# Performance work log

Hardware: AMD Instinct MI355X
Metric: run time of the kernel (lower is better)

The kernel has to match this reference:

```python
import jax, jax.numpy as jnp
import numpy as np

N_NODES = 100_000
N_EDGES = 1_600_000
RBF_DIM = 128
DIM = 64
N_CLUSTERS = 10
DIFF_RATE = 0.2


def softplus_sp(x):
    # torch.nn.Softplus(beta=0.5, threshold=14): (1/beta)*log(1+exp(beta*x)),
    # exact identity when beta*x > threshold
    bx = 0.5 * x
    return jnp.where(bx > 14.0, x, 2.0 * jnp.logaddexp(0.0, bx))


def setup_inputs() -> dict:
    key = jax.random.key(0)
    ks = jax.random.split(key, 9)
    rbf = jax.random.normal(ks[0], (N_EDGES, RBF_DIM), dtype=jnp.float32)
    new_node = jax.random.normal(ks[1], (N_NODES, DIM), dtype=jnp.float32)
    src = jax.random.randint(ks[2], (N_EDGES,), 0, N_NODES, dtype=jnp.int32)
    dst = jax.random.randint(ks[3], (N_EDGES,), 0, N_NODES, dtype=jnp.int32)
    cluster_id = jax.random.randint(ks[4], (N_NODES,), 0, N_CLUSTERS, dtype=jnp.int32)
    # intra-cluster edges always kept; inter-cluster (diff) edges sampled at diff_rate
    same = cluster_id[src] == cluster_id[dst]
    keep_diff = jax.random.uniform(ks[5], (N_EDGES,)) < DIFF_RATE
    edge_mask = same | ((~same) & keep_diff)
    # Linear params stored as [in, out]; equivalent to torch Linear weight.T
    W1 = jax.random.normal(ks[6], (RBF_DIM, DIM), dtype=jnp.float32) * 0.05
    b1 = jnp.zeros((DIM,), dtype=jnp.float32)
    W2 = jax.random.normal(ks[7], (DIM, DIM), dtype=jnp.float32) * 0.05
    b2 = jnp.zeros((DIM,), dtype=jnp.float32)
    return {"rbf": rbf, "new_node": new_node, "src": src, "dst": dst,
            "edge_mask": edge_mask, "W1": W1, "b1": b1, "W2": W2, "b2": b2}


def reference(rbf, new_node, src, dst, edge_mask, W1, b1, W2, b2):
    n_nodes = new_node.shape[0]
    # edge MLP applied to ALL edges (apply_edges runs on whole graph)
    h = softplus_sp(rbf @ W1 + b1) @ W2 + b2            # [E, dim]
    # gather src features, multiply by edge filter, mask to selected edges
    msg = jnp.where(edge_mask[:, None], new_node[src] * h, 0.0)  # [E, dim]
    # scatter-sum into destination nodes (nodes w/o messages get 0)
    out = jax.ops.segment_sum(msg, dst, num_segments=n_nodes)    # [N, dim]
    return out
```

## Files before the change

kernel.cpp:

```cpp
#include <hip/hip_runtime.h>
#include <hip/hip_bf16.h>

#define NN      100000
#define NE      1600000
#define RBF     128
#define DIM     64

__device__ __forceinline__ float lo_bf(unsigned int u) {
    union { unsigned int i; float f; } v; v.i = u << 16; return v.f;
}
__device__ __forceinline__ float hi_bf(unsigned int u) {
    union { unsigned int i; float f; } v; v.i = u & 0xffff0000u; return v.f;
}
__device__ __forceinline__ float us_bf(unsigned short u) {
    union { unsigned int i; float f; } v; v.i = ((unsigned int)u) << 16; return v.f;
}

__global__ void sniff_kernel(const unsigned int* __restrict__ rbf_raw,
                             const unsigned int* __restrict__ mask_raw,
                             int* __restrict__ flags)
{
    const int lane = threadIdx.x & 63;
    int fh = 0, mh = 0;
    for (int i = lane; i < 256; i += 64) {
        const unsigned int u = rbf_raw[i];
        if (((u >> 7) & 0xffu) >= 0x90u) fh = 1;
        if (mask_raw[i] > 1u) mh = 1;
    }
    const int fcnt = __popcll(__ballot(fh));
    const int mcnt = __popcll(__ballot(mh));
    if (lane == 0) {
        flags[0] = (fcnt >= 4) ? 1 : 0;
        flags[1] = (mcnt >= 4) ? 1 : 0;
    }
}

template <bool FP32>
__global__ __launch_bounds__(256, 2)
void edge_kernel(const void* __restrict__ rbf_v,
                 const void* __restrict__ nn_v,
                 const int*  __restrict__ src,
                 const int*  __restrict__ dst,
                 const void* __restrict__ mask_v,
                 const void* __restrict__ W1_v,
                 const void* __restrict__ b1_v,
                 const void* __restrict__ W2_v,
                 const void* __restrict__ b2_v,
                 const int*  __restrict__ flags,
                 float*      __restrict__ acc)
{
    if ((flags[0] != 0) != FP32) return;
    const int mask8 = flags[1];

    const int lane = threadIdx.x & 63;
    const int wib  = threadIdx.x >> 6;
    const int gw   = blockIdx.x * 4 + wib;
    const int nw   = gridDim.x * 4;

    float w1c[RBF];
    float w2c[DIM];
    float b1v, b2v;
    if constexpr (FP32) {
        const float* W1 = (const float*)W1_v;
        const float* W2 = (const float*)W2_v;
#pragma unroll
        for (int k = 0; k < RBF; ++k) w1c[k] = W1[k * DIM + lane];
#pragma unroll
        for (int j = 0; j < DIM; ++j) w2c[j] = W2[j * DIM + lane];
        b1v = ((const float*)b1_v)[lane];
        b2v = ((const float*)b2_v)[lane];
    } else {
        const unsigned short* W1 = (const unsigned short*)W1_v;
        const unsigned short* W2 = (const unsigned short*)W2_v;
#pragma unroll
        for (int k = 0; k < RBF; ++k) w1c[k] = us_bf(W1[k * DIM + lane]);
#pragma unroll
        for (int j = 0; j < DIM; ++j) w2c[j] = us_bf(W2[j * DIM + lane]);
        b1v = us_bf(((const unsigned short*)b1_v)[lane]);
        b2v = us_bf(((const unsigned short*)b2_v)[lane]);
    }

    __shared__ alignas(16) float sp_lds[4][DIM];
    float* myl = sp_lds[wib];

    for (int base = gw * 64; base < NE; base += nw * 64) {
        const int e_l = base + lane;
        int m_l;
        if (mask8) m_l = ((const unsigned char*)mask_v)[e_l];
        else       m_l = ((const int*)mask_v)[e_l];
        const int s_l = src[e_l];
        const int d_l = dst[e_l];
        unsigned long long bal = __ballot(m_l != 0);

        while (bal) {
            const int l = __ffsll((unsigned long long)bal) - 1;
            bal &= bal - 1;
            const int ee = __builtin_amdgcn_readfirstlane(base + l);
            const int s  = __shfl(s_l, l);
            const int d  = __shfl(d_l, l);

            float a0 = b1v, a1 = 0.f, a2 = 0.f, a3 = 0.f;
            if constexpr (FP32) {
                const float4* r = (const float4*)((const float*)rbf_v + (size_t)ee * RBF);
#pragma unroll
                for (int q = 0; q < RBF / 4; q += 4) {
                    const float4 v0 = r[q + 0], v1 = r[q + 1];
                    const float4 v2 = r[q + 2], v3 = r[q + 3];
                    a0 += v0.x*w1c[4*q+ 0] + v0.y*w1c[4*q+ 1] + v0.z*w1c[4*q+ 2] + v0.w*w1c[4*q+ 3];
                    a1 += v1.x*w1c[4*q+ 4] + v1.y*w1c[4*q+ 5] + v1.z*w1c[4*q+ 6] + v1.w*w1c[4*q+ 7];
                    a2 += v2.x*w1c[4*q+ 8] + v2.y*w1c[4*q+ 9] + v2.z*w1c[4*q+10] + v2.w*w1c[4*q+11];
                    a3 += v3.x*w1c[4*q+12] + v3.y*w1c[4*q+13] + v3.z*w1c[4*q+14] + v3.w*w1c[4*q+15];
                }
            } else {
                const unsigned int* r = (const unsigned int*)rbf_v + (size_t)ee * (RBF / 2);
#pragma unroll
                for (int k2 = 0; k2 < RBF / 2; k2 += 4) {
                    const unsigned int u0 = r[k2 + 0], u1 = r[k2 + 1];
                    const unsigned int u2 = r[k2 + 2], u3 = r[k2 + 3];
                    a0 += lo_bf(u0) * w1c[2*k2 + 0] + hi_bf(u0) * w1c[2*k2 + 1];
                    a1 += lo_bf(u1) * w1c[2*k2 + 2] + hi_bf(u1) * w1c[2*k2 + 3];
                    a2 += lo_bf(u2) * w1c[2*k2 + 4] + hi_bf(u2) * w1c[2*k2 + 5];
                    a3 += lo_bf(u3) * w1c[2*k2 + 6] + hi_bf(u3) * w1c[2*k2 + 7];
                }
            }
            const float x = (a0 + a1) + (a2 + a3);

            const float bx = 0.5f * x;
            float sp;
            if (bx > 14.0f) sp = x;
            else sp = 2.0f * (fmaxf(bx, 0.0f) + log1pf(__expf(-fabsf(bx))));

            myl[lane] = sp;
            __builtin_amdgcn_wave_barrier();
            const float4* spv = (const float4*)myl;
            float h0 = b2v, h1 = 0.f, h2 = 0.f, h3 = 0.f;
#pragma unroll
            for (int j4 = 0; j4 < DIM / 4; j4 += 4) {
                const float4 v0 = spv[j4 + 0], v1 = spv[j4 + 1];
                const float4 v2 = spv[j4 + 2], v3 = spv[j4 + 3];
                h0 += v0.x*w2c[4*j4+ 0] + v0.y*w2c[4*j4+ 1] + v0.z*w2c[4*j4+ 2] + v0.w*w2c[4*j4+ 3];
                h1 += v1.x*w2c[4*j4+ 4] + v1.y*w2c[4*j4+ 5] + v1.z*w2c[4*j4+ 6] + v1.w*w2c[4*j4+ 7];
                h2 += v2.x*w2c[4*j4+ 8] + v2.y*w2c[4*j4+ 9] + v2.z*w2c[4*j4+10] + v2.w*w2c[4*j4+11];
                h3 += v3.x*w2c[4*j4+12] + v3.y*w2c[4*j4+13] + v3.z*w2c[4*j4+14] + v3.w*w2c[4*j4+15];
            }
            const float h = (h0 + h1) + (h2 + h3);
            __builtin_amdgcn_wave_barrier();

            float nnv;
            if constexpr (FP32) nnv = ((const float*)nn_v)[(size_t)s * DIM + lane];
            else                nnv = us_bf(((const unsigned short*)nn_v)[(size_t)s * DIM + lane]);
            atomicAdd(&acc[(size_t)d * DIM + lane], nnv * h);
        }
    }
}

__global__ void finalize_kernel(const float* __restrict__ acc,
                                void* __restrict__ out,
                                const int* __restrict__ flags, int n)
{
    const int i = blockIdx.x * blockDim.x + threadIdx.x;
    if (i < n) {
        const float v = acc[i];
        if (flags[0]) ((float*)out)[i] = v;
        else          ((__hip_bfloat16*)out)[i] = __float2bfloat16(v);
    }
}

extern "C" void kernel_launch(void* const* d_in, const int* in_sizes, int n_in,
                              void* d_out, int out_size, void* d_ws, size_t ws_size,
                              hipStream_t stream)
{
    const void* rbf  = d_in[0];
    const void* nn   = d_in[1];
    const int*  src  = (const int*)d_in[2];
    const int*  dst  = (const int*)d_in[3];
    const void* mask = d_in[4];
    const void* W1   = d_in[5];
    const void* b1   = d_in[6];
    const void* W2   = d_in[7];
    const void* b2   = d_in[8];

    int*   flags = (int*)d_ws;
    float* acc   = (float*)d_ws + 64;

    hipMemsetAsync(acc, 0, (size_t)NN * DIM * sizeof(float), stream);
    sniff_kernel<<<1, 64, 0, stream>>>((const unsigned int*)rbf,
                                       (const unsigned int*)mask, flags);
    edge_kernel<true ><<<512, 256, 0, stream>>>(rbf, nn, src, dst, mask,
                                                W1, b1, W2, b2, flags, acc);
    edge_kernel<false><<<512, 256, 0, stream>>>(rbf, nn, src, dst, mask,
                                                W1, b1, W2, b2, flags, acc);
    finalize_kernel<<<((NN * DIM) + 255) / 256, 256, 0, stream>>>(
        acc, d_out, flags, NN * DIM);
}
```

Before: 1.730 ms.

## Compact masked edges and compute edge MLP one edge per lane with uniform weights

Adds a compaction pass that writes the indices of kept edges into a scratch list, so the edge kernel only visits masked-in edges in dense 64-edge tiles. The edge MLP changes from one edge per wave (weights held per lane in registers) to one edge per lane with 64-wide register accumulators, reading converted weights as wave-uniform loads and transposing through swizzled LDS between the two matmuls and before the scatter. This aims to remove serialized per-edge wave work and the cross-lane reductions. In exchange it needs large register arrays per lane, reads rbf rows in a strided per-lane pattern, and uses the output buffer as scratch before the finalize pass overwrites it.

Measured after the change: 1.608 ms. -7.0%, faster.

```diff
diff --git a/kernel.cpp b/kernel.cpp
--- a/kernel.cpp
+++ b/kernel.cpp
@@ -15,6 +15,10 @@
 __device__ __forceinline__ float us_bf(unsigned short u) {
     union { unsigned int i; float f; } v; v.i = ((unsigned int)u) << 16; return v.f;
 }
+
+#define FMA64(accv, rv, wrow) \
+    _Pragma("unroll") \
+    for (int j = 0; j < 64; ++j) (accv)[j] += (rv) * (wrow)[j];
 
 __global__ void sniff_kernel(const unsigned int* __restrict__ rbf_raw,
                              const unsigned int* __restrict__ mask_raw,
@@ -32,124 +36,186 @@
     if (lane == 0) {
         flags[0] = (fcnt >= 4) ? 1 : 0;
         flags[1] = (mcnt >= 4) ? 1 : 0;
+        flags[2] = 0;
+    }
+}
+
+__global__ void wconvert_kernel(const void* __restrict__ W1_v,
+                                const void* __restrict__ b1_v,
+                                const void* __restrict__ W2_v,
+                                const void* __restrict__ b2_v,
+                                const int* __restrict__ flags,
+                                float* __restrict__ wf)
+{
+    const int f32 = flags[0];
+    for (int i = blockIdx.x * blockDim.x + threadIdx.x; i < 12416;
+         i += gridDim.x * blockDim.x) {
+        float v;
+        if (i < 8192) {
+            v = f32 ? ((const float*)W1_v)[i] : us_bf(((const unsigned short*)W1_v)[i]);
+        } else if (i < 8256) {
+            const int j = i - 8192;
+            v = f32 ? ((const float*)b1_v)[j] : us_bf(((const unsigned short*)b1_v)[j]);
+        } else if (i < 12352) {
+            const int j = i - 8256;
+            v = f32 ? ((const float*)W2_v)[j] : us_bf(((const unsigned short*)W2_v)[j]);
+        } else {
+            const int j = i - 12352;
+            v = f32 ? ((const float*)b2_v)[j] : us_bf(((const unsigned short*)b2_v)[j]);
+        }
+        wf[i] = v;
+    }
+}
+
+__global__ void compact_kernel(const void* __restrict__ mask_v,
+                               const int* __restrict__ flags,
+                               int* __restrict__ kept,
+                               int* __restrict__ counter)
+{
+    const int mask8 = flags[1];
+    const int lane = threadIdx.x & 63;
+    const int gw = (blockIdx.x * blockDim.x + threadIdx.x) >> 6;
+    const int nw = (gridDim.x * blockDim.x) >> 6;
+    for (int base = gw * 64; base < NE; base += nw * 64) {
+        const int e = base + lane;
+        int m = 0;
+        if (e < NE)
+            m = mask8 ? (int)((const unsigned char*)mask_v)[e]
+                      : ((const int*)mask_v)[e];
+        const unsigned long long bal = __ballot(m != 0);
+        int wbase = 0;
+        if (lane == 0) {
+            const int cnt = (int)__popcll(bal);
+            if (cnt) wbase = atomicAdd(counter, cnt);
+        }
+        wbase = __shfl(wbase, 0);
+        if (m) {
+            const int pos = wbase + (int)__popcll(bal & ((1ull << lane) - 1ull));
+            kept[pos] = e;
+        }
     }
 }
 
 template <bool FP32>
-__global__ __launch_bounds__(256, 2)
+__global__ __launch_bounds__(128, 2)
 void edge_kernel(const void* __restrict__ rbf_v,
                  const void* __restrict__ nn_v,
                  const int*  __restrict__ src,
                  const int*  __restrict__ dst,
-                 const void* __restrict__ mask_v,
-                 const void* __restrict__ W1_v,
-                 const void* __restrict__ b1_v,
-                 const void* __restrict__ W2_v,
-                 const void* __restrict__ b2_v,
+                 const int*  __restrict__ kept,
+                 const float* __restrict__ wf,
                  const int*  __restrict__ flags,
-                 float*      __restrict__ acc)
+                 float* __restrict__ acc)
 {
     if ((flags[0] != 0) != FP32) return;
-    const int mask8 = flags[1];
+    const int total = flags[2];
+    if (total <= 0) return;
+
+    const float* __restrict__ w1f = wf;
+    const float* __restrict__ b1f = wf + 8192;
+    const float* __restrict__ w2f = wf + 8256;
+    const float* __restrict__ b2f = wf + 12352;
 
     const int lane = threadIdx.x & 63;
     const int wib  = threadIdx.x >> 6;
-    const int gw   = blockIdx.x * 4 + wib;
-    const int nw   = gridDim.x * 4;
-
-    float w1c[RBF];
-    float w2c[DIM];
-    float b1v, b2v;
-    if constexpr (FP32) {
-        const float* W1 = (const float*)W1_v;
-        const float* W2 = (const float*)W2_v;
-#pragma unroll
-        for (int k = 0; k < RBF; ++k) w1c[k] = W1[k * DIM + lane];
-#pragma unroll
-        for (int j = 0; j < DIM; ++j) w2c[j] = W2[j * DIM + lane];
-        b1v = ((const float*)b1_v)[lane];
-        b2v = ((const float*)b2_v)[lane];
-    } else {
-        const unsigned short* W1 = (const unsigned short*)W1_v;
-        const unsigned short* W2 = (const unsigned short*)W2_v;
-#pragma unroll
-        for (int k = 0; k < RBF; ++k) w1c[k] = us_bf(W1[k * DIM + lane]);
-#pragma unroll
-        for (int j = 0; j < DIM; ++j) w2c[j] = us_bf(W2[j * DIM + lane]);
-        b1v = us_bf(((const unsigned short*)b1_v)[lane]);
-        b2v = us_bf(((const unsigned short*)b2_v)[lane]);
-    }
-
-    __shared__ alignas(16) float sp_lds[4][DIM];
-    float* myl = sp_lds[wib];
-
-    for (int base = gw * 64; base < NE; base += nw * 64) {
-        const int e_l = base + lane;
-        int m_l;
-        if (mask8) m_l = ((const unsigned char*)mask_v)[e_l];
-        else       m_l = ((const int*)mask_v)[e_l];
-        const int s_l = src[e_l];
-        const int d_l = dst[e_l];
-        unsigned long long bal = __ballot(m_l != 0);
-
-        while (bal) {
-            const int l = __ffsll((unsigned long long)bal) - 1;
-            bal &= bal - 1;
-            const int ee = __builtin_amdgcn_readfirstlane(base + l);
-            const int s  = __shfl(s_l, l);
-            const int d  = __shfl(d_l, l);
-
-            float a0 = b1v, a1 = 0.f, a2 = 0.f, a3 = 0.f;
-            if constexpr (FP32) {
-                const float4* r = (const float4*)((const float*)rbf_v + (size_t)ee * RBF);
-#pragma unroll
-                for (int q = 0; q < RBF / 4; q += 4) {
-                    const float4 v0 = r[q + 0], v1 = r[q + 1];
-                    const float4 v2 = r[q + 2], v3 = r[q + 3];
-                    a0 += v0.x*w1c[4*q+ 0] + v0.y*w1c[4*q+ 1] + v0.z*w1c[4*q+ 2] + v0.w*w1c[4*q+ 3];
-                    a1 += v1.x*w1c[4*q+ 4] + v1.y*w1c[4*q+ 5] + v1.z*w1c[4*q+ 6] + v1.w*w1c[4*q+ 7];
-                    a2 += v2.x*w1c[4*q+ 8] + v2.y*w1c[4*q+ 9] + v2.z*w1c[4*q+10] + v2.w*w1c[4*q+11];
-                    a3 += v3.x*w1c[4*q+12] + v3.y*w1c[4*q+13] + v3.z*w1c[4*q+14] + v3.w*w1c[4*q+15];
-                }
-            } else {
-                const unsigned int* r = (const unsigned int*)rbf_v + (size_t)ee * (RBF / 2);
-#pragma unroll
-                for (int k2 = 0; k2 < RBF / 2; k2 += 4) {
-                    const unsigned int u0 = r[k2 + 0], u1 = r[k2 + 1];
-                    const unsigned int u2 = r[k2 + 2], u3 = r[k2 + 3];
-                    a0 += lo_bf(u0) * w1c[2*k2 + 0] + hi_bf(u0) * w1c[2*k2 + 1];
-                    a1 += lo_bf(u1) * w1c[2*k2 + 2] + hi_bf(u1) * w1c[2*k2 + 3];
-                    a2 += lo_bf(u2) * w1c[2*k2 + 4] + hi_bf(u2) * w1c[2*k2 + 5];
-                    a3 += lo_bf(u3) * w1c[2*k2 + 6] + hi_bf(u3) * w1c[2*k2 + 7];
-                }
+    const int gw   = blockIdx.x * 2 + wib;
+    const int nw   = gridDim.x * 2;
+
+    __shared__ float tb[2][64 * 64];
+    float* __restrict__ tbw = tb[wib];
+
+    const int ntiles = (total + 63) >> 6;
+    for (int t = gw; t < ntiles; t += nw) {
+        const int i0 = t << 6;
+        const int valid = min(64, total - i0);
+        const int ii = i0 + min(lane, valid - 1);
+        const int eid = kept[ii];
+        const int s_l = src[eid];
+        const int d_l = dst[eid];
+
+        float x[64];
+#pragma unroll
+        for (int j = 0; j < 64; ++j) x[j] = b1f[j];
+
+        if constexpr (FP32) {
+            const float4* __restrict__ rr =
+                (const float4*)((const float*)rbf_v + (size_t)eid * RBF);
+            for (int k4 = 0; k4 < RBF / 4; ++k4) {
+                const float4 r = rr[k4];
+                const float* __restrict__ w = w1f + k4 * 256;
+                FMA64(x, r.x, w);
+                FMA64(x, r.y, w + 64);
+                FMA64(x, r.z, w + 128);
+                FMA64(x, r.w, w + 192);
             }
-            const float x = (a0 + a1) + (a2 + a3);
-
-            const float bx = 0.5f * x;
-            float sp;
-            if (bx > 14.0f) sp = x;
-            else sp = 2.0f * (fmaxf(bx, 0.0f) + log1pf(__expf(-fabsf(bx))));
-
-            myl[lane] = sp;
-            __builtin_amdgcn_wave_barrier();
-            const float4* spv = (const float4*)myl;
-            float h0 = b2v, h1 = 0.f, h2 = 0.f, h3 = 0.f;
-#pragma unroll
-            for (int j4 = 0; j4 < DIM / 4; j4 += 4) {
-                const float4 v0 = spv[j4 + 0], v1 = spv[j4 + 1];
-                const float4 v2 = spv[j4 + 2], v3 = spv[j4 + 3];
-                h0 += v0.x*w2c[4*j4+ 0] + v0.y*w2c[4*j4+ 1] + v0.z*w2c[4*j4+ 2] + v0.w*w2c[4*j4+ 3];
-                h1 += v1.x*w2c[4*j4+ 4] + v1.y*w2c[4*j4+ 5] + v1.z*w2c[4*j4+ 6] + v1.w*w2c[4*j4+ 7];
-                h2 += v2.x*w2c[4*j4+ 8] + v2.y*w2c[4*j4+ 9] + v2.z*w2c[4*j4+10] + v2.w*w2c[4*j4+11];
-                h3 += v3.x*w2c[4*j4+12] + v3.y*w2c[4*j4+13] + v3.z*w2c[4*j4+14] + v3.w*w2c[4*j4+15];
+        } else {
+            const uint4* __restrict__ rr =
+                (const uint4*)((const unsigned short*)rbf_v + (size_t)eid * RBF);
+            for (int k8 = 0; k8 < RBF / 8; ++k8) {
+                const uint4 u = rr[k8];
+                const float* __restrict__ w = w1f + k8 * 512;
+                const float r0 = lo_bf(u.x), r1 = hi_bf(u.x);
+                const float r2 = lo_bf(u.y), r3 = hi_bf(u.y);
+                const float r4 = lo_bf(u.z), r5 = hi_bf(u.z);
+                const float r6 = lo_bf(u.w), r7 = hi_bf(u.w);
+                FMA64(x, r0, w);
+                FMA64(x, r1, w + 64);
+                FMA64(x, r2, w + 128);
+                FMA64(x, r3, w + 192);
+                FMA64(x, r4, w + 256);
+                FMA64(x, r5, w + 320);
+                FMA64(x, r6, w + 384);
+                FMA64(x, r7, w + 448);
             }
-            const float h = (h0 + h1) + (h2 + h3);
-            __builtin_amdgcn_wave_barrier();
-
+        }
+
+#pragma unroll
+        for (int j = 0; j < 64; ++j) {
+            const float bx = 0.5f * x[j];
+            const float sp = 2.0f * (fmaxf(bx, 0.0f) + log1pf(__expf(-fabsf(bx))));
+            x[j] = (bx > 14.0f) ? x[j] : sp;
+        }
+
+#pragma unroll
+        for (int c4 = 0; c4 < 16; ++c4) {
+            const int sw = (c4 ^ (lane & 15)) << 2;
+            float4 v;
+            v.x = x[c4 * 4 + 0]; v.y = x[c4 * 4 + 1];
+            v.z = x[c4 * 4 + 2]; v.w = x[c4 * 4 + 3];
+            *(float4*)&tbw[(lane << 6) + sw] = v;
+        }
+
+        float h[64];
+#pragma unroll
+        for (int j = 0; j < 64; ++j) h[j] = b2f[j];
+        for (int j4 = 0; j4 < 16; ++j4) {
+            const int sw = (j4 ^ (lane & 15)) << 2;
+            const float4 s4 = *(const float4*)&tbw[(lane << 6) + sw];
+            const float* __restrict__ w = w2f + j4 * 256;
+            FMA64(h, s4.x, w);
+            FMA64(h, s4.y, w + 64);
+            FMA64(h, s4.z, w + 128);
+            FMA64(h, s4.w, w + 192);
+        }
+
+#pragma unroll
+        for (int c4 = 0; c4 < 16; ++c4) {
+            const int sw = (c4 ^ (lane & 15)) << 2;
+            float4 v;
+            v.x = h[c4 * 4 + 0]; v.y = h[c4 * 4 + 1];
+            v.z = h[c4 * 4 + 2]; v.w = h[c4 * 4 + 3];
+            *(float4*)&tbw[(lane << 6) + sw] = v;
+        }
+
+        for (int e = 0; e < valid; ++e) {
+            const int s = __shfl(s_l, e);
+            const int d = __shfl(d_l, e);
+            const int sw = ((((lane >> 2) ^ (e & 15)) << 2) | (lane & 3));
+            const float hv = tbw[(e << 6) + sw];
             float nnv;
             if constexpr (FP32) nnv = ((const float*)nn_v)[(size_t)s * DIM + lane];
             else                nnv = us_bf(((const unsigned short*)nn_v)[(size_t)s * DIM + lane]);
-            atomicAdd(&acc[(size_t)d * DIM + lane], nnv * h);
+            atomicAdd(&acc[(size_t)d * DIM + lane], nnv * hv);
         }
     }
 }
@@ -183,13 +249,16 @@
     int*   flags = (int*)d_ws;
     float* acc   = (float*)d_ws + 64;
 
+    int*   kept = (int*)d_out;
+    float* wf   = (float*)((char*)d_out + (size_t)NE * sizeof(int));
+
     hipMemsetAsync(acc, 0, (size_t)NN * DIM * sizeof(float), stream);
     sniff_kernel<<<1, 64, 0, stream>>>((const unsigned int*)rbf,
                                        (const unsigned int*)mask, flags);
-    edge_kernel<true ><<<512, 256, 0, stream>>>(rbf, nn, src, dst, mask,
-                                                W1, b1, W2, b2, flags, acc);
-    edge_kernel<false><<<512, 256, 0, stream>>>(rbf, nn, src, dst, mask,
-                                                W1, b1, W2, b2, flags, acc);
+    wconvert_kernel<<<32, 256, 0, stream>>>(W1, b1, W2, b2, flags, wf);
+    compact_kernel<<<512, 256, 0, stream>>>(mask, flags, kept, flags + 2);
+    edge_kernel<true ><<<2048, 128, 0, stream>>>(rbf, nn, src, dst, kept, wf, flags, acc);
+    edge_kernel<false><<<2048, 128, 0, stream>>>(rbf, nn, src, dst, kept, wf, flags, acc);
     finalize_kernel<<<((NN * DIM) + 255) / 256, 256, 0, stream>>>(
         acc, d_out, flags, NN * DIM);
 }
```
